# Performance work log

Measured on AMD Instinct MI355X. Metric: run time of the kernel, lower is better.

The kernel has to match this reference:

```python
import jax, jax.numpy as jnp
import numpy as np

INPUT_DIM = 128
OUTPUT_DIM = 64
EMBED_DIM = 3
B, S = 16, 2048
EPS = 1e-6


def setup_inputs() -> dict:
    key = jax.random.key(0)
    ks = jax.random.split(key, 8)
    scale = 0.05
    return {
        "x": jax.random.normal(ks[0], (B, S, INPUT_DIM), dtype=jnp.float32),
        "threshold": jnp.asarray(0.1, dtype=jnp.float32),
        "w1": jax.random.normal(ks[1], (INPUT_DIM, 2 * EMBED_DIM), dtype=jnp.float32) * scale,
        "b1": jnp.zeros((2 * EMBED_DIM,), dtype=jnp.float32),
        "w2": jax.random.normal(ks[2], (2 * EMBED_DIM, EMBED_DIM), dtype=jnp.float32) * scale,
        "b2": jnp.zeros((EMBED_DIM,), dtype=jnp.float32),
        "w3": jax.random.normal(ks[3], (4, OUTPUT_DIM), dtype=jnp.float32) * scale,
        "b3": jnp.zeros((OUTPUT_DIM,), dtype=jnp.float32),
    }


def reference(x, threshold, w1, b1, w2, b2, w3, b3):
    # phase-space embedding: Linear -> ReLU -> Linear   [B,S,E]
    h = jnp.maximum(x @ w1 + b1, 0.0) @ w2 + b2
    Bsz, Slen, _ = h.shape

    # pairwise euclidean distances (torch.cdist) per batch element [B,S,S]
    sq = jnp.sum(h * h, axis=-1)                         # [B,S]
    d2 = sq[:, :, None] + sq[:, None, :] - 2.0 * jnp.einsum('bse,bte->bst', h, h)
    dist = jnp.sqrt(jnp.maximum(d2, 0.0))

    # per-sample threshold = sigmoid(theta) * max(dist)
    thr = jax.nn.sigmoid(threshold) * jnp.max(dist, axis=(1, 2), keepdims=True)
    R = (dist < thr).astype(h.dtype)                     # recurrence matrix [B,S,S]

    total = jnp.sum(R, axis=(1, 2))                      # [B]
    rr = total / (Slen * Slen)                           # recurrence rate

    # sum of super-diagonals with offsets 1..min(S,10)-1
    idx = jnp.arange(Slen)
    off = idx[None, :] - idx[:, None]
    dmask = ((off >= 1) & (off <= min(Slen, 10) - 1)).astype(h.dtype)  # [S,S]
    diag_structures = jnp.einsum('bst,st->b', R, dmask)
    det = diag_structures / (total + EPS)

    # vertical structures: per column (over rows, axis=1), count runs of length >= 2.
    # a run of length>=2 starts at row i iff R[i]=1, R[i-1]=0 (or i=0), R[i+1]=1.
    prev = jnp.pad(R[:, :-1, :], ((0, 0), (1, 0), (0, 0)))
    nxt = jnp.pad(R[:, 1:, :], ((0, 0), (0, 1), (0, 0)))
    vert_structures = jnp.sum(R * (1.0 - prev) * nxt, axis=(1, 2))
    lam = vert_structures / (total + EPS)

    # 'entropy' term as written in the original (R is 0/1 valued)
    entr = -jnp.sum(R * jnp.log(R + EPS), axis=(1, 2))

    metrics = jnp.stack([rr, det, lam, entr], axis=-1)   # [B,4]
    return jnp.maximum(metrics @ w3 + b3, 0.0)           # [B,output_dim]
```

## Files before the change

### kernel.cpp

```cpp
#include <hip/hip_runtime.h>
#include <math.h>

#define B_ 16
#define S_ 2048
#define IN_DIM 128
#define E2 6
#define E_ 3
#define OUT_DIM 64


__global__ __launch_bounds__(256) void embed_kernel(
    const float* __restrict__ x, const float* __restrict__ w1,
    const float* __restrict__ b1, const float* __restrict__ w2,
    const float* __restrict__ b2, float* __restrict__ hws,
    int* __restrict__ acc)
{
    if (blockIdx.x == 0 && threadIdx.x < 64) acc[threadIdx.x] = 0;
    int wave = threadIdx.x >> 6;
    int lane = threadIdx.x & 63;
    int row  = blockIdx.x * 4 + wave;
    const float2* x2 = (const float2*)(x + (size_t)row * IN_DIM);
    float2 xv = x2[lane];
    const float* w1a = w1 + (2 * lane) * E2;
    float a[E2];
#pragma unroll
    for (int q = 0; q < E2; ++q)
        a[q] = xv.x * w1a[q] + xv.y * w1a[E2 + q];
#pragma unroll
    for (int q = 0; q < E2; ++q) {
#pragma unroll
        for (int off = 32; off >= 1; off >>= 1)
            a[q] += __shfl_xor(a[q], off, 64);
    }
    if (lane == 0) {
        float r[E2];
#pragma unroll
        for (int q = 0; q < E2; ++q) r[q] = fmaxf(a[q] + b1[q], 0.f);
        float h[E_];
#pragma unroll
        for (int e = 0; e < E_; ++e) {
            float s = b2[e];
#pragma unroll
            for (int q = 0; q < E2; ++q) s += r[q] * w2[q * E_ + e];
            h[e] = s;
        }
        float sq = h[0] * h[0] + h[1] * h[1] + h[2] * h[2];
        ((float4*)hws)[row] = make_float4(h[0], h[1], h[2], sq);
    }
}

__global__ __launch_bounds__(256) void max_kernel(
    const float4* __restrict__ h4, int* __restrict__ acc)
{
    int bid = blockIdx.x;
    int b  = bid >> 6;
    int cb = (bid >> 5) & 1;
    int rb = bid & 31;
    int r0 = rb * 64;
    int c0 = cb * 1024;
    if (r0 > c0 + 1023) return;
    const float4* hb = h4 + (size_t)b * S_;
    __shared__ float4 sh[64];
    if (threadIdx.x < 64) sh[threadIdx.x] = hb[r0 + threadIdx.x];
    float4 hj[4];
#pragma unroll
    for (int c = 0; c < 4; ++c) hj[c] = hb[c0 + c * 256 + threadIdx.x];
    __syncthreads();
    float mc[4] = {-1e30f, -1e30f, -1e30f, -1e30f};
#pragma unroll 4
    for (int k = 0; k < 64; ++k) {
        float4 rv = sh[k];
#pragma unroll
        for (int c = 0; c < 4; ++c) {
            float dot = fmaf(hj[c].x, rv.x, fmaf(hj[c].y, rv.y, hj[c].z * rv.z));
            mc[c] = fmaxf(mc[c], fmaf(-2.f, dot, rv.w));
        }
    }
    float m = fmaxf(fmaxf(mc[0] + hj[0].w, mc[1] + hj[1].w),
                    fmaxf(mc[2] + hj[2].w, mc[3] + hj[3].w));
    m = fmaxf(m, 0.f);
#pragma unroll
    for (int off = 32; off >= 1; off >>= 1)
        m = fmaxf(m, __shfl_xor(m, off, 64));
    __shared__ float wmax[4];
    int lane = threadIdx.x & 63, wave = threadIdx.x >> 6;
    if (lane == 0) wmax[wave] = m;
    __syncthreads();
    if (threadIdx.x == 0) {
        float mm = fmaxf(fmaxf(wmax[0], wmax[1]), fmaxf(wmax[2], wmax[3]));
        atomicMax(&acc[b * 4 + 0], __float_as_int(mm));
    }
}

__global__ __launch_bounds__(256) void stats_kernel(
    const float4* __restrict__ h4, const float* __restrict__ theta,
    int* __restrict__ acc)
{
    int bid = blockIdx.x;
    int b  = bid >> 6;
    int cb = (bid >> 5) & 1;
    int rb = bid & 31;
    int r0 = rb * 64;
    int c0 = cb * 1024;
    const float4* hb = h4 + (size_t)b * S_;
    __shared__ float4 sh[66];
    if (threadIdx.x < 66) {
        int r = r0 - 1 + threadIdx.x;
        r = r < 0 ? 0 : (r >= S_ ? S_ - 1 : r);
        sh[threadIdx.x] = hb[r];
    }
    float4 hj[4];
#pragma unroll
    for (int c = 0; c < 4; ++c) hj[c] = hb[c0 + c * 256 + threadIdx.x];
    __syncthreads();
    float maxd2 = __int_as_float(acc[b * 4 + 0]);
    float sig   = 1.f / (1.f + expf(-theta[0]));
    float thr2  = sig * sig * maxd2;
    float thrc[4];
#pragma unroll
    for (int c = 0; c < 4; ++c) thrc[c] = thr2 - hj[c].w;

    unsigned m0[4] = {0u,0u,0u,0u}, m1[4] = {0u,0u,0u,0u};
#pragma unroll 4
    for (int k = 0; k < 32; ++k) {
        float4 rv = sh[1 + k];
        unsigned bitk = 1u << k;
#pragma unroll
        for (int c = 0; c < 4; ++c) {
            float dot = fmaf(hj[c].x, rv.x, fmaf(hj[c].y, rv.y, hj[c].z * rv.z));
            m0[c] |= (fmaf(-2.f, dot, rv.w) < thrc[c]) ? bitk : 0u;
        }
    }
#pragma unroll 4
    for (int k = 0; k < 32; ++k) {
        float4 rv = sh[33 + k];
        unsigned bitk = 1u << k;
#pragma unroll
        for (int c = 0; c < 4; ++c) {
            float dot = fmaf(hj[c].x, rv.x, fmaf(hj[c].y, rv.y, hj[c].z * rv.z));
            m1[c] |= (fmaf(-2.f, dot, rv.w) < thrc[c]) ? bitk : 0u;
        }
    }

    int total = 0, diag = 0, vert = 0;
#pragma unroll
    for (int c = 0; c < 4; ++c) {
        int j = c0 + c * 256 + threadIdx.x;
        unsigned long long m = ((unsigned long long)m1[c] << 32) | m0[c];
        total += __popcll(m);
        float4 pr = sh[0], nx = sh[65];
        float dotp = fmaf(hj[c].x, pr.x, fmaf(hj[c].y, pr.y, hj[c].z * pr.z));
        float dotn = fmaf(hj[c].x, nx.x, fmaf(hj[c].y, nx.y, hj[c].z * nx.z));
        unsigned long long prevbit =
            (r0 > 0) ? ((fmaf(-2.f, dotp, pr.w) < thrc[c]) ? 1ull : 0ull) : 0ull;
        unsigned long long nextbit =
            (r0 + 64 < S_) ? ((fmaf(-2.f, dotn, nx.w) < thrc[c]) ? 1ull : 0ull) : 0ull;
        unsigned long long notprev = ~((m << 1) | prevbit);
        vert += __popcll(m & notprev & ((m >> 1) | (nextbit << 63)));
        int lo = j - 9 - r0, hi = j - 1 - r0;
        if (hi >= 0 && lo <= 63) {
            int l = lo < 0 ? 0 : lo;
            int h = hi > 63 ? 63 : hi;
            unsigned long long bandm = ((1ull << (h - l + 1)) - 1ull) << l;
            diag += __popcll(m & bandm);
        }
    }

#pragma unroll
    for (int off = 32; off >= 1; off >>= 1) {
        total += __shfl_xor(total, off, 64);
        diag  += __shfl_xor(diag,  off, 64);
        vert  += __shfl_xor(vert,  off, 64);
    }
    __shared__ int wsum[4][3];
    int lane = threadIdx.x & 63, wave = threadIdx.x >> 6;
    if (lane == 0) { wsum[wave][0] = total; wsum[wave][1] = diag; wsum[wave][2] = vert; }
    __syncthreads();
    if (threadIdx.x == 0) {
        int t = 0, d = 0, v = 0;
#pragma unroll
        for (int w = 0; w < 4; ++w) { t += wsum[w][0]; d += wsum[w][1]; v += wsum[w][2]; }
        atomicAdd(&acc[b * 4 + 1], t);
        atomicAdd(&acc[b * 4 + 2], d);
        atomicAdd(&acc[b * 4 + 3], v);
    }
}

__global__ void finalize_kernel(const int* __restrict__ acc,
    const float* __restrict__ w3, const float* __restrict__ b3,
    float* __restrict__ out)
{
    int idx = blockIdx.x * 256 + threadIdx.x;
    if (idx >= B_ * OUT_DIM) return;
    int b = idx >> 6, o = idx & 63;
    float total = (float)acc[b * 4 + 1];
    float diag  = (float)acc[b * 4 + 2];
    float vert  = (float)acc[b * 4 + 3];
    float rr  = total / (float)(S_ * S_);
    float det = diag / (total + 1e-6f);
    float lam = vert / (total + 1e-6f);
    float entr = -total * logf(1.0f + 1e-6f);
    float r = b3[o] + rr  * w3[0 * OUT_DIM + o]
                    + det * w3[1 * OUT_DIM + o]
                    + lam * w3[2 * OUT_DIM + o]
                    + entr * w3[3 * OUT_DIM + o];
    out[idx] = fmaxf(r, 0.f);
}

extern "C" void kernel_launch(void* const* d_in, const int* in_sizes, int n_in,
                              void* d_out, int out_size, void* d_ws, size_t ws_size,
                              hipStream_t stream) {
    const float* x     = (const float*)d_in[0];
    const float* theta = (const float*)d_in[1];
    const float* w1    = (const float*)d_in[2];
    const float* b1    = (const float*)d_in[3];
    const float* w2    = (const float*)d_in[4];
    const float* b2    = (const float*)d_in[5];
    const float* w3    = (const float*)d_in[6];
    const float* b3    = (const float*)d_in[7];
    float* out = (float*)d_out;
    float* hws = (float*)d_ws;
    int* acc = (int*)((char*)d_ws + (size_t)B_ * S_ * 4 * sizeof(float));

    hipLaunchKernelGGL(embed_kernel, dim3(B_ * S_ / 4), dim3(256), 0, stream,
                       x, w1, b1, w2, b2, hws, acc);
    hipLaunchKernelGGL(max_kernel, dim3(B_ * 64), dim3(256), 0, stream,
                       (const float4*)hws, acc);
    hipLaunchKernelGGL(stats_kernel, dim3(B_ * 64), dim3(256), 0, stream,
                       (const float4*)hws, theta, acc);
    hipLaunchKernelGGL(finalize_kernel, dim3(4), dim3(256), 0, stream, acc, w3, b3, out);
}
```

Before: 122.7 us.

## Widen per-thread column tiles and fold -2 scaling into shared row data

The max and stats kernels now give each block all 2048 columns of a 64-row strip, so each thread handles 8 columns and the grid is half as large. Row vectors are pre-scaled by -2 when staged into shared memory, so each distance test is three chained FMAs instead of multiply plus FMAs. The stats kernel builds a single 64-bit mask per column and packs the diag and vert counts into one int for the shuffle reduction. In exchange the max kernel drops its triangular block skip and now computes the full matrix, the smaller grid of 512 blocks lowers occupancy, and the packed counts rely on per-wave values fitting in 16 bits.

```diff
diff --git a/kernel.cpp b/kernel.cpp
--- a/kernel.cpp
+++ b/kernel.cpp
@@ -53,31 +53,36 @@
     const float4* __restrict__ h4, int* __restrict__ acc)
 {
     int bid = blockIdx.x;
-    int b  = bid >> 6;
-    int cb = (bid >> 5) & 1;
+    int b  = bid >> 5;
     int rb = bid & 31;
     int r0 = rb * 64;
-    int c0 = cb * 1024;
-    if (r0 > c0 + 1023) return;
     const float4* hb = h4 + (size_t)b * S_;
     __shared__ float4 sh[64];
-    if (threadIdx.x < 64) sh[threadIdx.x] = hb[r0 + threadIdx.x];
-    float4 hj[4];
-#pragma unroll
-    for (int c = 0; c < 4; ++c) hj[c] = hb[c0 + c * 256 + threadIdx.x];
-    __syncthreads();
-    float mc[4] = {-1e30f, -1e30f, -1e30f, -1e30f};
-#pragma unroll 4
+    if (threadIdx.x < 64) {
+        float4 rv = hb[r0 + threadIdx.x];
+        sh[threadIdx.x] = make_float4(-2.f * rv.x, -2.f * rv.y, -2.f * rv.z, rv.w);
+    }
+    float4 hj[8];
+#pragma unroll
+    for (int c = 0; c < 8; ++c) hj[c] = hb[c * 256 + threadIdx.x];
+    __syncthreads();
+    float mc[8];
+#pragma unroll
+    for (int c = 0; c < 8; ++c) mc[c] = -1e30f;
+#pragma unroll 2
     for (int k = 0; k < 64; ++k) {
         float4 rv = sh[k];
 #pragma unroll
-        for (int c = 0; c < 4; ++c) {
-            float dot = fmaf(hj[c].x, rv.x, fmaf(hj[c].y, rv.y, hj[c].z * rv.z));
-            mc[c] = fmaxf(mc[c], fmaf(-2.f, dot, rv.w));
-        }
-    }
-    float m = fmaxf(fmaxf(mc[0] + hj[0].w, mc[1] + hj[1].w),
-                    fmaxf(mc[2] + hj[2].w, mc[3] + hj[3].w));
+        for (int c = 0; c < 8; ++c) {
+            float t = fmaf(hj[c].x, rv.x,
+                      fmaf(hj[c].y, rv.y,
+                      fmaf(hj[c].z, rv.z, rv.w)));
+            mc[c] = fmaxf(mc[c], t);
+        }
+    }
+    float m = -1e30f;
+#pragma unroll
+    for (int c = 0; c < 8; ++c) m = fmaxf(m, mc[c] + hj[c].w);
     m = fmaxf(m, 0.f);
 #pragma unroll
     for (int off = 32; off >= 1; off >>= 1)
@@ -97,64 +102,54 @@
     int* __restrict__ acc)
 {
     int bid = blockIdx.x;
-    int b  = bid >> 6;
-    int cb = (bid >> 5) & 1;
+    int b  = bid >> 5;
     int rb = bid & 31;
     int r0 = rb * 64;
-    int c0 = cb * 1024;
     const float4* hb = h4 + (size_t)b * S_;
     __shared__ float4 sh[66];
     if (threadIdx.x < 66) {
         int r = r0 - 1 + threadIdx.x;
         r = r < 0 ? 0 : (r >= S_ ? S_ - 1 : r);
-        sh[threadIdx.x] = hb[r];
-    }
-    float4 hj[4];
-#pragma unroll
-    for (int c = 0; c < 4; ++c) hj[c] = hb[c0 + c * 256 + threadIdx.x];
+        float4 rv = hb[r];
+        sh[threadIdx.x] = make_float4(-2.f * rv.x, -2.f * rv.y, -2.f * rv.z, rv.w);
+    }
+    float4 hj[8];
+#pragma unroll
+    for (int c = 0; c < 8; ++c) hj[c] = hb[c * 256 + threadIdx.x];
     __syncthreads();
     float maxd2 = __int_as_float(acc[b * 4 + 0]);
     float sig   = 1.f / (1.f + expf(-theta[0]));
     float thr2  = sig * sig * maxd2;
-    float thrc[4];
-#pragma unroll
-    for (int c = 0; c < 4; ++c) thrc[c] = thr2 - hj[c].w;
-
-    unsigned m0[4] = {0u,0u,0u,0u}, m1[4] = {0u,0u,0u,0u};
-#pragma unroll 4
-    for (int k = 0; k < 32; ++k) {
+    float thrc[8];
+#pragma unroll
+    for (int c = 0; c < 8; ++c) thrc[c] = thr2 - hj[c].w;
+
+    unsigned long long mk[8];
+#pragma unroll
+    for (int c = 0; c < 8; ++c) mk[c] = 0ull;
+#pragma unroll 2
+    for (int k = 0; k < 64; ++k) {
         float4 rv = sh[1 + k];
-        unsigned bitk = 1u << k;
-#pragma unroll
-        for (int c = 0; c < 4; ++c) {
-            float dot = fmaf(hj[c].x, rv.x, fmaf(hj[c].y, rv.y, hj[c].z * rv.z));
-            m0[c] |= (fmaf(-2.f, dot, rv.w) < thrc[c]) ? bitk : 0u;
-        }
-    }
-#pragma unroll 4
-    for (int k = 0; k < 32; ++k) {
-        float4 rv = sh[33 + k];
-        unsigned bitk = 1u << k;
-#pragma unroll
-        for (int c = 0; c < 4; ++c) {
-            float dot = fmaf(hj[c].x, rv.x, fmaf(hj[c].y, rv.y, hj[c].z * rv.z));
-            m1[c] |= (fmaf(-2.f, dot, rv.w) < thrc[c]) ? bitk : 0u;
+#pragma unroll
+        for (int c = 0; c < 8; ++c) {
+            float t = fmaf(hj[c].x, rv.x,
+                      fmaf(hj[c].y, rv.y,
+                      fmaf(hj[c].z, rv.z, rv.w)));
+            mk[c] |= (t < thrc[c]) ? (1ull << k) : 0ull;
         }
     }
 
     int total = 0, diag = 0, vert = 0;
-#pragma unroll
-    for (int c = 0; c < 4; ++c) {
-        int j = c0 + c * 256 + threadIdx.x;
-        unsigned long long m = ((unsigned long long)m1[c] << 32) | m0[c];
+    float4 pr = sh[0], nx = sh[65];
+#pragma unroll
+    for (int c = 0; c < 8; ++c) {
+        int j = c * 256 + threadIdx.x;
+        unsigned long long m = mk[c];
         total += __popcll(m);
-        float4 pr = sh[0], nx = sh[65];
-        float dotp = fmaf(hj[c].x, pr.x, fmaf(hj[c].y, pr.y, hj[c].z * pr.z));
-        float dotn = fmaf(hj[c].x, nx.x, fmaf(hj[c].y, nx.y, hj[c].z * nx.z));
-        unsigned long long prevbit =
-            (r0 > 0) ? ((fmaf(-2.f, dotp, pr.w) < thrc[c]) ? 1ull : 0ull) : 0ull;
-        unsigned long long nextbit =
-            (r0 + 64 < S_) ? ((fmaf(-2.f, dotn, nx.w) < thrc[c]) ? 1ull : 0ull) : 0ull;
+        float tp = fmaf(hj[c].x, pr.x, fmaf(hj[c].y, pr.y, fmaf(hj[c].z, pr.z, pr.w)));
+        float tn = fmaf(hj[c].x, nx.x, fmaf(hj[c].y, nx.y, fmaf(hj[c].z, nx.z, nx.w)));
+        unsigned long long prevbit = (r0 > 0) ? ((tp < thrc[c]) ? 1ull : 0ull) : 0ull;
+        unsigned long long nextbit = (r0 + 64 < S_) ? ((tn < thrc[c]) ? 1ull : 0ull) : 0ull;
         unsigned long long notprev = ~((m << 1) | prevbit);
         vert += __popcll(m & notprev & ((m >> 1) | (nextbit << 63)));
         int lo = j - 9 - r0, hi = j - 1 - r0;
@@ -166,20 +161,24 @@
         }
     }
 
+    int dv = (diag << 16) | vert;
 #pragma unroll
     for (int off = 32; off >= 1; off >>= 1) {
         total += __shfl_xor(total, off, 64);
-        diag  += __shfl_xor(diag,  off, 64);
-        vert  += __shfl_xor(vert,  off, 64);
-    }
-    __shared__ int wsum[4][3];
+        dv    += __shfl_xor(dv,    off, 64);
+    }
+    __shared__ int wsum[4][2];
     int lane = threadIdx.x & 63, wave = threadIdx.x >> 6;
-    if (lane == 0) { wsum[wave][0] = total; wsum[wave][1] = diag; wsum[wave][2] = vert; }
+    if (lane == 0) { wsum[wave][0] = total; wsum[wave][1] = dv; }
     __syncthreads();
     if (threadIdx.x == 0) {
         int t = 0, d = 0, v = 0;
 #pragma unroll
-        for (int w = 0; w < 4; ++w) { t += wsum[w][0]; d += wsum[w][1]; v += wsum[w][2]; }
+        for (int w = 0; w < 4; ++w) {
+            t += wsum[w][0];
+            d += wsum[w][1] >> 16;
+            v += wsum[w][1] & 0xFFFF;
+        }
         atomicAdd(&acc[b * 4 + 1], t);
         atomicAdd(&acc[b * 4 + 2], d);
         atomicAdd(&acc[b * 4 + 3], v);
@@ -224,9 +223,9 @@
 
     hipLaunchKernelGGL(embed_kernel, dim3(B_ * S_ / 4), dim3(256), 0, stream,
                        x, w1, b1, w2, b2, hws, acc);
-    hipLaunchKernelGGL(max_kernel, dim3(B_ * 64), dim3(256), 0, stream,
+    hipLaunchKernelGGL(max_kernel, dim3(B_ * 32), dim3(256), 0, stream,
                        (const float4*)hws, acc);
-    hipLaunchKernelGGL(stats_kernel, dim3(B_ * 64), dim3(256), 0, stream,
+    hipLaunchKernelGGL(stats_kernel, dim3(B_ * 32), dim3(256), 0, stream,
                        (const float4*)hws, theta, acc);
     hipLaunchKernelGGL(finalize_kernel, dim3(4), dim3(256), 0, stream, acc, w3, b3, out);
 }
```

Result: faster. 116.3 us (-5.2%).
